# Optimization experiments

Measured on AMD Instinct MI355X. Metric: run time of the kernel, lower is better.

## Reference

```python
import jax, jax.numpy as jnp
import numpy as np

B, T, D = 2, 1024, 128
NEG_INF = -1e9


def setup_inputs() -> dict:
    key = jax.random.key(0)
    k_h, k_m, k_w = jax.random.split(key, 3)
    h = jax.random.normal(k_h, (B, T, D), dtype=jnp.float32)
    mask = jax.random.uniform(k_m, (B, T)) < 0.9  # bool [B, T]
    w = jax.random.normal(k_w, (D,), dtype=jnp.float32) * (1.0 / np.sqrt(D))  # Linear(dim,1,bias=False)
    return {"h": h, "mask": mask, "w": w}


def reference(h, mask, w):
    # wj[b, j] = W(h[b, j]) : score column scale, independent of i
    wj = jnp.einsum("btd,d->bt", h, w)  # [B, T]
    # pairwise L1 distance: dist[b, i, j] = sum_d |h[b,i,d] - h[b,j,d]|
    dist = jnp.abs(h[:, :, None, :] - h[:, None, :, :]).sum(-1)  # [B, T, T]
    score = -wj[:, None, :] * dist  # [B, T, T]
    score = jnp.where(mask[:, None, :], score, NEG_INF)
    alpha = jax.nn.softmax(score, axis=-1)  # [B, T, T]
    ctx = jnp.einsum("bij,bjd->bid", alpha, h)  # [B, T, D]
    return jnp.concatenate([h, ctx], axis=-1)  # [B, T, 2D]
```

## Files before the change

### kernel.cpp

```cpp
#include <hip/hip_runtime.h>
#include <math.h>

#define TT 1024
#define DD 128

static constexpr float kNegInf = -1e9f;

typedef __fp16 h2 __attribute__((ext_vector_type(2)));

__device__ __forceinline__ unsigned int pk16(float a, float b) {
  h2 v = __builtin_amdgcn_cvt_pkrtz(a, b);
  return __builtin_bit_cast(unsigned int, v);
}
__device__ __forceinline__ float dot2f(unsigned int a, unsigned int b, float c) {
#if __has_builtin(__builtin_amdgcn_fdot2)
  return __builtin_amdgcn_fdot2(__builtin_bit_cast(h2, a),
                                __builtin_bit_cast(h2, b), c, false);
#else
  h2 av = __builtin_bit_cast(h2, a), bv = __builtin_bit_cast(h2, b);
  return c + (float)av.x * (float)bv.x + (float)av.y * (float)bv.y;
#endif
}

__global__ __launch_bounds__(256) void k_prep(const float* __restrict__ h,
                                              const float* __restrict__ w,
                                              const int* __restrict__ mk,
                                              float* __restrict__ hTf,
                                              unsigned int* __restrict__ hT16,
                                              float* __restrict__ swj,
                                              float* __restrict__ bias) {
  __shared__ __align__(16) float tile[32][132];
  __shared__ float wred[32][8];
  const int b  = blockIdx.x >> 5;
  const int jt = blockIdx.x & 31;
  const int tid = threadIdx.x;
  const float4* src = (const float4*)h + (size_t)(b * TT + jt * 32) * 32;
#pragma unroll
  for (int k = 0; k < 4; ++k) {
    int idx = k * 256 + tid;
    float4 v = src[idx];
    int j = idx >> 5, c = idx & 31;
    *((float4*)&tile[j][c * 4]) = v;
  }
  __syncthreads();
#pragma unroll
  for (int k = 0; k < 4; ++k) {
    int idx = k * 256 + tid;
    int d = idx >> 3, jq = idx & 7;
    float4 v = {tile[jq * 4 + 0][d], tile[jq * 4 + 1][d],
                tile[jq * 4 + 2][d], tile[jq * 4 + 3][d]};
    *(float4*)&hTf[(size_t)(b * DD + d) * TT + jt * 32 + jq * 4] = v;
  }
#pragma unroll
  for (int k = 0; k < 2; ++k) {
    int idx = k * 256 + tid;
    int jp = idx >> 5, dq = idx & 31;
    uint4 wv;
    wv.x = pk16(tile[jp * 2][dq * 4 + 0], tile[jp * 2 + 1][dq * 4 + 0]);
    wv.y = pk16(tile[jp * 2][dq * 4 + 1], tile[jp * 2 + 1][dq * 4 + 1]);
    wv.z = pk16(tile[jp * 2][dq * 4 + 2], tile[jp * 2 + 1][dq * 4 + 2]);
    wv.w = pk16(tile[jp * 2][dq * 4 + 3], tile[jp * 2 + 1][dq * 4 + 3]);
    *(uint4*)&hT16[((size_t)(b * 512 + jt * 16 + jp)) * DD + dq * 4] = wv;
  }
  {
    const int j = tid & 31, dg = tid >> 5;
    float p = 0.f;
#pragma unroll
    for (int e = 0; e < 16; e += 4) {
      float4 hv = *(const float4*)&tile[j][dg * 16 + e];
      float4 wv = *(const float4*)&w[dg * 16 + e];
      p += hv.x * wv.x + hv.y * wv.y + hv.z * wv.z + hv.w * wv.w;
    }
    wred[j][dg] = p;
  }
  __syncthreads();
  if (tid < 32) {
    const int row = b * TT + jt * 32 + tid;
    float a = 0.f;
#pragma unroll
    for (int e = 0; e < 8; ++e) a += wred[tid][e];
    const bool ok = (mk[row] != 0);
    swj[row]  = ok ? -a : 0.f;
    bias[row] = ok ? 0.f : kNegInf;
  }
}

__global__ __launch_bounds__(256, 2) void k_fused(
    const float* __restrict__ h, const float* __restrict__ hTf,
    const unsigned int* __restrict__ hT16,
    const float* __restrict__ swj, const float* __restrict__ bias,
    float* __restrict__ out) {
  __shared__ __align__(16) float A_lds[4][DD];
  __shared__ __align__(16) unsigned int Pt[512][4];
  __shared__ __align__(16) float ctxp[4][4][DD];
  __shared__ float redm[4][4];
  __shared__ float redl[4][4];

  const int tid  = threadIdx.x;
  const int lane = tid & 63;
  const int wv   = tid >> 6;
  const int b    = blockIdx.x >> 8;
  const int row0 = (blockIdx.x & 255) * 4;

  {
    const float2 v = *(const float2*)(h + ((size_t)b * TT + row0) * DD + tid * 2);
    *(float2*)&A_lds[0][tid * 2] = v;
  }
  __syncthreads();

  const int j = tid * 4;
  const float* Bb = hTf + (size_t)b * DD * TT + j;
  float acc[4][4];
#pragma unroll
  for (int u = 0; u < 4; ++u)
#pragma unroll
    for (int r = 0; r < 4; ++r) acc[u][r] = 0.f;

#define LOADB4(B, s) {                                     \
    B[0] = *(const float4*)(Bb + (size_t)((s) * 4 + 0) * TT); \
    B[1] = *(const float4*)(Bb + (size_t)((s) * 4 + 1) * TT); \
    B[2] = *(const float4*)(Bb + (size_t)((s) * 4 + 2) * TT); \
    B[3] = *(const float4*)(Bb + (size_t)((s) * 4 + 3) * TT); }

#define COMP4(B, s) {                                                  \
    _Pragma("unroll") for (int r = 0; r < 4; ++r) {                    \
      const float4 Ar = *(const float4*)&A_lds[r][(s) * 4];            \
      _Pragma("unroll") for (int e = 0; e < 4; ++e) {                  \
        const float a = (e == 0) ? Ar.x : (e == 1) ? Ar.y              \
                        : (e == 2) ? Ar.z : Ar.w;                      \
        acc[0][r] += fabsf(a - B[e].x);                                \
        acc[1][r] += fabsf(a - B[e].y);                                \
        acc[2][r] += fabsf(a - B[e].z);                                \
        acc[3][r] += fabsf(a - B[e].w);                                \
      } } }

  {
    float4 B0[4], B1[4];
    LOADB4(B0, 0);
#pragma unroll 1
    for (int s = 0; s < 16; ++s) {
      LOADB4(B1, 2 * s + 1);
      COMP4(B0, 2 * s);
      if (s < 15) LOADB4(B0, 2 * s + 2);
      COMP4(B1, 2 * s + 1);
    }
  }

  const float4 swv = *(const float4*)(swj + (size_t)b * TT + j);
  const float4 bvv = *(const float4*)(bias + (size_t)b * TT + j);
  float sc[4][4];
#pragma unroll
  for (int r = 0; r < 4; ++r) {
    sc[0][r] = fmaf(swv.x, acc[0][r], bvv.x);
    sc[1][r] = fmaf(swv.y, acc[1][r], bvv.y);
    sc[2][r] = fmaf(swv.z, acc[2][r], bvv.z);
    sc[3][r] = fmaf(swv.w, acc[3][r], bvv.w);
  }

  {
    float mr[4];
#pragma unroll
    for (int r = 0; r < 4; ++r) {
      float m0 = fmaxf(fmaxf(sc[0][r], sc[1][r]), fmaxf(sc[2][r], sc[3][r]));
#pragma unroll
      for (int off = 32; off; off >>= 1) m0 = fmaxf(m0, __shfl_xor(m0, off));
      mr[r] = m0;
    }
    if (lane == 0) {
#pragma unroll
      for (int r = 0; r < 4; ++r) redm[wv][r] = mr[r];
    }
  }
  __syncthreads();
  float M[4];
#pragma unroll
  for (int r = 0; r < 4; ++r)
    M[r] = fmaxf(fmaxf(redm[0][r], redm[1][r]),
                 fmaxf(redm[2][r], redm[3][r]));

  {
    float p[4][4];
    float ls[4] = {0.f, 0.f, 0.f, 0.f};
#pragma unroll
    for (int u = 0; u < 4; ++u)
#pragma unroll
      for (int r = 0; r < 4; ++r) {
        p[u][r] = __expf(sc[u][r] - M[r]);
        ls[r] += p[u][r];
      }
    uint4 w0 = {pk16(p[0][0], p[1][0]), pk16(p[0][1], p[1][1]),
                pk16(p[0][2], p[1][2]), pk16(p[0][3], p[1][3])};
    uint4 w1 = {pk16(p[2][0], p[3][0]), pk16(p[2][1], p[3][1]),
                pk16(p[2][2], p[3][2]), pk16(p[2][3], p[3][3])};
    *(uint4*)&Pt[tid * 2 + 0][0] = w0;
    *(uint4*)&Pt[tid * 2 + 1][0] = w1;
#pragma unroll
    for (int r = 0; r < 4; ++r) {
#pragma unroll
      for (int off = 32; off; off >>= 1) ls[r] += __shfl_xor(ls[r], off);
    }
    if (lane == 0) {
#pragma unroll
      for (int r = 0; r < 4; ++r) redl[wv][r] = ls[r];
    }
  }
  __syncthreads();

  const int dp = tid & 63;
  const int s  = tid >> 6;
  const unsigned int* Vp =
      hT16 + ((size_t)(b * 512 + s * 128)) * DD + dp * 2;
  float cx[4][2];
#pragma unroll
  for (int r = 0; r < 4; ++r) { cx[r][0] = 0.f; cx[r][1] = 0.f; }
#pragma unroll 4
  for (int q = 0; q < 128; ++q) {
    const uint4 P = *(const uint4*)&Pt[s * 128 + q][0];
    const uint2 V = *(const uint2*)(Vp + (size_t)q * DD);
    cx[0][0] = dot2f(P.x, V.x, cx[0][0]); cx[0][1] = dot2f(P.x, V.y, cx[0][1]);
    cx[1][0] = dot2f(P.y, V.x, cx[1][0]); cx[1][1] = dot2f(P.y, V.y, cx[1][1]);
    cx[2][0] = dot2f(P.z, V.x, cx[2][0]); cx[2][1] = dot2f(P.z, V.y, cx[2][1]);
    cx[3][0] = dot2f(P.w, V.x, cx[3][0]); cx[3][1] = dot2f(P.w, V.y, cx[3][1]);
  }
#pragma unroll
  for (int r = 0; r < 4; ++r)
    *(float2*)&ctxp[s][r][dp * 2] = make_float2(cx[r][0], cx[r][1]);
  __syncthreads();

#pragma unroll
  for (int k = 0; k < 2; ++k) {
    const int idx = tid + k * 256;
    const int r = idx >> 7, d = idx & 127;
    const float L = redl[0][r] + redl[1][r] + redl[2][r] + redl[3][r];
    const float c = (ctxp[0][r][d] + ctxp[1][r][d]) +
                    (ctxp[2][r][d] + ctxp[3][r][d]);
    const size_t row = (size_t)blockIdx.x * 4 + r;
    out[row * 256 + d]       = A_lds[r][d];
    out[row * 256 + 128 + d] = c / L;
  }
}

extern "C" void kernel_launch(void* const* d_in, const int* in_sizes, int n_in,
                              void* d_out, int out_size, void* d_ws, size_t ws_size,
                              hipStream_t stream) {
  const float* h  = (const float*)d_in[0];
  const int*   mk = (const int*)d_in[1];
  const float* w  = (const float*)d_in[2];
  float* out = (float*)d_out;

  char* ws = (char*)d_ws;
  float*        swj  = (float*)ws;
  float*        bias = (float*)(ws + 8192);
  float*        hTf  = (float*)(ws + 16384);
  unsigned int* hT16 = (unsigned int*)(ws + 16384 + 1048576);

  hipLaunchKernelGGL(k_prep,  dim3(64),  dim3(256), 0, stream,
                     h, w, mk, hTf, hT16, swj, bias);
  hipLaunchKernelGGL(k_fused, dim3(512), dim3(256), 0, stream,
                     h, hTf, hT16, swj, bias, out);
}
```

Baseline: 43.43 us.

## Split key dimension across two blocks with flash-style partial softmax merge

Each fused block now handles half of the key range (512 columns) for 4 query rows, with threads split into two row pairs. It writes partial context sums and per-row (max, sum) to workspace, and a new merge kernel rescales and combines the halves. Launch bounds rise to allow four blocks per CU. This doubles the grid to 1024 blocks for better occupancy on the 256-CU device, at the cost of an extra launch and a global round trip for partials.

```diff
diff --git a/kernel.cpp b/kernel.cpp
--- a/kernel.cpp
+++ b/kernel.cpp
@@ -85,22 +85,24 @@
   }
 }
 
-__global__ __launch_bounds__(256, 2) void k_fused(
+__global__ __launch_bounds__(256, 4) void k_fused(
     const float* __restrict__ h, const float* __restrict__ hTf,
     const unsigned int* __restrict__ hT16,
     const float* __restrict__ swj, const float* __restrict__ bias,
-    float* __restrict__ out) {
+    float* __restrict__ ctxpart, float2* __restrict__ mlpart) {
   __shared__ __align__(16) float A_lds[4][DD];
-  __shared__ __align__(16) unsigned int Pt[512][4];
+  __shared__ __align__(16) unsigned int Pt[256][4];
   __shared__ __align__(16) float ctxp[4][4][DD];
-  __shared__ float redm[4][4];
-  __shared__ float redl[4][4];
+  __shared__ float redm[4][2];
+  __shared__ float redl[4][2];
 
   const int tid  = threadIdx.x;
   const int lane = tid & 63;
   const int wv   = tid >> 6;
-  const int b    = blockIdx.x >> 8;
-  const int row0 = (blockIdx.x & 255) * 4;
+  const int rg   = blockIdx.x & 511;
+  const int jh   = blockIdx.x >> 9;
+  const int b    = rg >> 8;
+  const int row0 = (rg & 255) * 4;
 
   {
     const float2 v = *(const float2*)(h + ((size_t)b * TT + row0) * DD + tid * 2);
@@ -108,31 +110,35 @@
   }
   __syncthreads();
 
-  const int j = tid * 4;
+  const int jq = tid & 127;
+  const int rp = tid >> 7;
+  const int j  = jh * 512 + jq * 4;
   const float* Bb = hTf + (size_t)b * DD * TT + j;
-  float acc[4][4];
-#pragma unroll
-  for (int u = 0; u < 4; ++u)
-#pragma unroll
-    for (int r = 0; r < 4; ++r) acc[u][r] = 0.f;
-
-#define LOADB4(B, s) {                                     \
+  const float* Ar0 = &A_lds[rp * 2][0];
+  const float* Ar1 = &A_lds[rp * 2 + 1][0];
+  float acc[4][2];
+#pragma unroll
+  for (int u = 0; u < 4; ++u) { acc[u][0] = 0.f; acc[u][1] = 0.f; }
+
+#define LOADB4(B, s) {                                        \
     B[0] = *(const float4*)(Bb + (size_t)((s) * 4 + 0) * TT); \
     B[1] = *(const float4*)(Bb + (size_t)((s) * 4 + 1) * TT); \
     B[2] = *(const float4*)(Bb + (size_t)((s) * 4 + 2) * TT); \
     B[3] = *(const float4*)(Bb + (size_t)((s) * 4 + 3) * TT); }
 
 #define COMP4(B, s) {                                                  \
-    _Pragma("unroll") for (int r = 0; r < 4; ++r) {                    \
-      const float4 Ar = *(const float4*)&A_lds[r][(s) * 4];            \
-      _Pragma("unroll") for (int e = 0; e < 4; ++e) {                  \
-        const float a = (e == 0) ? Ar.x : (e == 1) ? Ar.y              \
-                        : (e == 2) ? Ar.z : Ar.w;                      \
-        acc[0][r] += fabsf(a - B[e].x);                                \
-        acc[1][r] += fabsf(a - B[e].y);                                \
-        acc[2][r] += fabsf(a - B[e].z);                                \
-        acc[3][r] += fabsf(a - B[e].w);                                \
-      } } }
+    const float4 A0 = *(const float4*)(Ar0 + (s) * 4);                 \
+    const float4 A1 = *(const float4*)(Ar1 + (s) * 4);                 \
+    _Pragma("unroll") for (int e = 0; e < 4; ++e) {                    \
+      const float a0 = (e == 0) ? A0.x : (e == 1) ? A0.y               \
+                       : (e == 2) ? A0.z : A0.w;                       \
+      const float a1 = (e == 0) ? A1.x : (e == 1) ? A1.y               \
+                       : (e == 2) ? A1.z : A1.w;                       \
+      acc[0][0] += fabsf(a0 - B[e].x); acc[0][1] += fabsf(a1 - B[e].x);\
+      acc[1][0] += fabsf(a0 - B[e].y); acc[1][1] += fabsf(a1 - B[e].y);\
+      acc[2][0] += fabsf(a0 - B[e].z); acc[2][1] += fabsf(a1 - B[e].z);\
+      acc[3][0] += fabsf(a0 - B[e].w); acc[3][1] += fabsf(a1 - B[e].w);\
+    } }
 
   {
     float4 B0[4], B1[4];
@@ -148,74 +154,74 @@
 
   const float4 swv = *(const float4*)(swj + (size_t)b * TT + j);
   const float4 bvv = *(const float4*)(bias + (size_t)b * TT + j);
-  float sc[4][4];
-#pragma unroll
-  for (int r = 0; r < 4; ++r) {
-    sc[0][r] = fmaf(swv.x, acc[0][r], bvv.x);
-    sc[1][r] = fmaf(swv.y, acc[1][r], bvv.y);
-    sc[2][r] = fmaf(swv.z, acc[2][r], bvv.z);
-    sc[3][r] = fmaf(swv.w, acc[3][r], bvv.w);
-  }
-
-  {
-    float mr[4];
-#pragma unroll
-    for (int r = 0; r < 4; ++r) {
-      float m0 = fmaxf(fmaxf(sc[0][r], sc[1][r]), fmaxf(sc[2][r], sc[3][r]));
+  float sc[4][2];
+  sc[0][0] = fmaf(swv.x, acc[0][0], bvv.x);
+  sc[0][1] = fmaf(swv.x, acc[0][1], bvv.x);
+  sc[1][0] = fmaf(swv.y, acc[1][0], bvv.y);
+  sc[1][1] = fmaf(swv.y, acc[1][1], bvv.y);
+  sc[2][0] = fmaf(swv.z, acc[2][0], bvv.z);
+  sc[2][1] = fmaf(swv.z, acc[2][1], bvv.z);
+  sc[3][0] = fmaf(swv.w, acc[3][0], bvv.w);
+  sc[3][1] = fmaf(swv.w, acc[3][1], bvv.w);
+
+  {
+    float mm[2];
+#pragma unroll
+    for (int rr = 0; rr < 2; ++rr) {
+      float m0 = fmaxf(fmaxf(sc[0][rr], sc[1][rr]),
+                       fmaxf(sc[2][rr], sc[3][rr]));
 #pragma unroll
       for (int off = 32; off; off >>= 1) m0 = fmaxf(m0, __shfl_xor(m0, off));
-      mr[r] = m0;
-    }
-    if (lane == 0) {
-#pragma unroll
-      for (int r = 0; r < 4; ++r) redm[wv][r] = mr[r];
-    }
-  }
-  __syncthreads();
-  float M[4];
-#pragma unroll
-  for (int r = 0; r < 4; ++r)
-    M[r] = fmaxf(fmaxf(redm[0][r], redm[1][r]),
-                 fmaxf(redm[2][r], redm[3][r]));
-
-  {
-    float p[4][4];
-    float ls[4] = {0.f, 0.f, 0.f, 0.f};
+      mm[rr] = m0;
+    }
+    if (lane == 0) { redm[wv][0] = mm[0]; redm[wv][1] = mm[1]; }
+  }
+  __syncthreads();
+  float M[2];
+  M[0] = fmaxf(redm[rp * 2][0], redm[rp * 2 + 1][0]);
+  M[1] = fmaxf(redm[rp * 2][1], redm[rp * 2 + 1][1]);
+
+  {
+    float p[4][2];
+    float ls[2] = {0.f, 0.f};
 #pragma unroll
     for (int u = 0; u < 4; ++u)
 #pragma unroll
-      for (int r = 0; r < 4; ++r) {
-        p[u][r] = __expf(sc[u][r] - M[r]);
-        ls[r] += p[u][r];
+      for (int rr = 0; rr < 2; ++rr) {
+        p[u][rr] = __expf(sc[u][rr] - M[rr]);
+        ls[rr] += p[u][rr];
       }
-    uint4 w0 = {pk16(p[0][0], p[1][0]), pk16(p[0][1], p[1][1]),
-                pk16(p[0][2], p[1][2]), pk16(p[0][3], p[1][3])};
-    uint4 w1 = {pk16(p[2][0], p[3][0]), pk16(p[2][1], p[3][1]),
-                pk16(p[2][2], p[3][2]), pk16(p[2][3], p[3][3])};
-    *(uint4*)&Pt[tid * 2 + 0][0] = w0;
-    *(uint4*)&Pt[tid * 2 + 1][0] = w1;
-#pragma unroll
-    for (int r = 0; r < 4; ++r) {
-#pragma unroll
-      for (int off = 32; off; off >>= 1) ls[r] += __shfl_xor(ls[r], off);
-    }
-    if (lane == 0) {
-#pragma unroll
-      for (int r = 0; r < 4; ++r) redl[wv][r] = ls[r];
-    }
-  }
-  __syncthreads();
+    Pt[jq * 2 + 0][rp * 2 + 0] = pk16(p[0][0], p[1][0]);
+    Pt[jq * 2 + 1][rp * 2 + 0] = pk16(p[2][0], p[3][0]);
+    Pt[jq * 2 + 0][rp * 2 + 1] = pk16(p[0][1], p[1][1]);
+    Pt[jq * 2 + 1][rp * 2 + 1] = pk16(p[2][1], p[3][1]);
+#pragma unroll
+    for (int rr = 0; rr < 2; ++rr) {
+#pragma unroll
+      for (int off = 32; off; off >>= 1) ls[rr] += __shfl_xor(ls[rr], off);
+    }
+    if (lane == 0) { redl[wv][0] = ls[0]; redl[wv][1] = ls[1]; }
+  }
+  __syncthreads();
+
+  if (tid < 4) {
+    const int r = tid;
+    const int w0 = (r >> 1) * 2, rr = r & 1;
+    const float Mr = fmaxf(redm[w0][rr], redm[w0 + 1][rr]);
+    const float Lr = redl[w0][rr] + redl[w0 + 1][rr];
+    mlpart[jh * 2048 + rg * 4 + r] = make_float2(Mr, Lr);
+  }
 
   const int dp = tid & 63;
   const int s  = tid >> 6;
   const unsigned int* Vp =
-      hT16 + ((size_t)(b * 512 + s * 128)) * DD + dp * 2;
+      hT16 + ((size_t)(b * 512 + jh * 256 + s * 64)) * DD + dp * 2;
   float cx[4][2];
 #pragma unroll
   for (int r = 0; r < 4; ++r) { cx[r][0] = 0.f; cx[r][1] = 0.f; }
 #pragma unroll 4
-  for (int q = 0; q < 128; ++q) {
-    const uint4 P = *(const uint4*)&Pt[s * 128 + q][0];
+  for (int q = 0; q < 64; ++q) {
+    const uint4 P = *(const uint4*)&Pt[s * 64 + q][0];
     const uint2 V = *(const uint2*)(Vp + (size_t)q * DD);
     cx[0][0] = dot2f(P.x, V.x, cx[0][0]); cx[0][1] = dot2f(P.x, V.y, cx[0][1]);
     cx[1][0] = dot2f(P.y, V.x, cx[1][0]); cx[1][1] = dot2f(P.y, V.y, cx[1][1]);
@@ -231,13 +237,27 @@
   for (int k = 0; k < 2; ++k) {
     const int idx = tid + k * 256;
     const int r = idx >> 7, d = idx & 127;
-    const float L = redl[0][r] + redl[1][r] + redl[2][r] + redl[3][r];
-    const float c = (ctxp[0][r][d] + ctxp[1][r][d]) +
-                    (ctxp[2][r][d] + ctxp[3][r][d]);
-    const size_t row = (size_t)blockIdx.x * 4 + r;
-    out[row * 256 + d]       = A_lds[r][d];
-    out[row * 256 + 128 + d] = c / L;
-  }
+    ctxpart[((size_t)(jh * 2048 + rg * 4 + r)) * DD + d] =
+        (ctxp[0][r][d] + ctxp[1][r][d]) + (ctxp[2][r][d] + ctxp[3][r][d]);
+  }
+}
+
+__global__ __launch_bounds__(256) void k_merge(const float* __restrict__ h,
+                                               const float* __restrict__ ctxpart,
+                                               const float2* __restrict__ mlpart,
+                                               float* __restrict__ out) {
+  const int row = blockIdx.x * 2 + (threadIdx.x >> 7);
+  const int d   = threadIdx.x & 127;
+
+  const float2 ml0 = mlpart[row];
+  const float2 ml1 = mlpart[2048 + row];
+  const float M  = fmaxf(ml0.x, ml1.x);
+  const float w0 = __expf(ml0.x - M), w1 = __expf(ml1.x - M);
+  const float L  = fmaf(ml0.y, w0, ml1.y * w1);
+  const float c  = ctxpart[(size_t)row * DD + d] * w0 +
+                   ctxpart[(size_t)(2048 + row) * DD + d] * w1;
+  out[(size_t)row * 256 + d]       = h[(size_t)row * DD + d];
+  out[(size_t)row * 256 + 128 + d] = c / L;
 }
 
 extern "C" void kernel_launch(void* const* d_in, const int* in_sizes, int n_in,
@@ -253,9 +273,13 @@
   float*        bias = (float*)(ws + 8192);
   float*        hTf  = (float*)(ws + 16384);
   unsigned int* hT16 = (unsigned int*)(ws + 16384 + 1048576);
-
-  hipLaunchKernelGGL(k_prep,  dim3(64),  dim3(256), 0, stream,
+  float*  ctxpart = (float*)(ws + 16384 + 1048576 + 524288);
+  float2* mlpart  = (float2*)(ws + 16384 + 1048576 + 524288 + 2097152);
+
+  hipLaunchKernelGGL(k_prep,  dim3(64),   dim3(256), 0, stream,
                      h, w, mk, hTf, hT16, swj, bias);
-  hipLaunchKernelGGL(k_fused, dim3(512), dim3(256), 0, stream,
-                     h, hTf, hT16, swj, bias, out);
-}
+  hipLaunchKernelGGL(k_fused, dim3(1024), dim3(256), 0, stream,
+                     h, hTf, hT16, swj, bias, ctxpart, mlpart);
+  hipLaunchKernelGGL(k_merge, dim3(1024), dim3(256), 0, stream,
+                     h, ctxpart, mlpart, out);
+}
```

New measurement: 44.34 us. +2.1%, slower.
